# Performance work log

Hardware: AMD Instinct MI355X
Metric: run time of the kernel (lower is better)

## Reference

```python
import jax, jax.numpy as jnp
import numpy as np

D_MODEL = 1024
NUM_HEADS = 16
HEAD_SIZE = D_MODEL // NUM_HEADS


def setup_inputs() -> dict:
    key = jax.random.key(0)
    ks = jax.random.split(key, 11)
    B, S, D = 4, 2048, D_MODEL
    scale = 1.0 / np.sqrt(D)
    inp = {
        "queries": jax.random.normal(ks[0], (B, S, D), jnp.float32),
        "keys": jax.random.normal(ks[1], (B, S, D), jnp.float32),
        "values": jax.random.normal(ks[2], (B, S, D), jnp.float32),
        "W_Q": jax.random.normal(ks[3], (D, D), jnp.float32) * scale,
        "b_Q": jax.random.normal(ks[4], (D,), jnp.float32) * 0.01,
        "W_K": jax.random.normal(ks[5], (D, D), jnp.float32) * scale,
        "b_K": jax.random.normal(ks[6], (D,), jnp.float32) * 0.01,
        "W_V": jax.random.normal(ks[7], (D, D), jnp.float32) * scale,
        "b_V": jax.random.normal(ks[8], (D,), jnp.float32) * 0.01,
        "W_O": jax.random.normal(ks[9], (D, D), jnp.float32) * scale,
        "b_O": jax.random.normal(ks[10], (D,), jnp.float32) * 0.01,
    }
    return inp


def _split_heads(x):
    B, S, D = x.shape
    return x.reshape(B, S, NUM_HEADS, HEAD_SIZE).transpose(0, 2, 1, 3)  # (B,H,S,hd)


def reference(queries, keys, values, W_Q, b_Q, W_K, b_K, W_V, b_V, W_O, b_O):
    # Linear projections (torch Linear: x @ W^T + b; here W stored as (D,D) used directly)
    q = _split_heads(queries @ W_Q + b_Q)  # (B,H,S,hd)
    k = _split_heads(keys @ W_K + b_K)
    v = _split_heads(values @ W_V + b_V)

    S = q.shape[2]
    scores = jnp.einsum("bhqd,bhkd->bhqk", q, k) / jnp.sqrt(jnp.float32(HEAD_SIZE))
    causal = jnp.tril(jnp.ones((S, S), dtype=bool))  # True where attention allowed
    scores = jnp.where(causal, scores, -jnp.inf)
    attn = jax.nn.softmax(scores, axis=-1)  # (B,H,S,S)

    ctx = jnp.einsum("bhqk,bhkd->bhqd", attn, v)  # (B,H,S,hd)
    B = ctx.shape[0]
    ctx = ctx.transpose(0, 2, 1, 3).reshape(B, S, D_MODEL)  # merge heads
    out = ctx @ W_O + b_O
    return out, jax.lax.stop_gradient(attn)
```

## Files before the change

### kernel.cpp

```cpp
#include <hip/hip_runtime.h>
#include <hip/hip_bf16.h>
#include <math.h>

#define D_MODEL 1024
#define NUM_HEADS 16
#define HEAD_SIZE 64
#define SEQ 2048
#define BATCH 4
#define M_PROJ (BATCH * SEQ)

typedef __attribute__((ext_vector_type(8))) short bf16x8;
typedef __attribute__((ext_vector_type(4))) float f32x4;

__device__ inline float bf2f(ushort u) {
  return __uint_as_float(((unsigned int)u) << 16);
}
__device__ inline ushort f2bf(float x) {
  unsigned int b = __float_as_uint(x);
  b += 0x7fffu + ((b >> 16) & 1u);
  return (ushort)(b >> 16);
}

__device__ inline void gload_lds16(const void* g, void* l) {
  __builtin_amdgcn_global_load_lds(
      (const __attribute__((address_space(1))) void*)g,
      (__attribute__((address_space(3))) void*)l, 16, 0, 0);
}

__global__ __launch_bounds__(256) void split_kernel(
    const float* __restrict__ in, ushort* __restrict__ hi,
    ushort* __restrict__ lo, int n4) {
  for (int i = blockIdx.x * 256 + threadIdx.x; i < n4; i += gridDim.x * 256) {
    float4 v = reinterpret_cast<const float4*>(in)[i];
    const float xs[4] = {v.x, v.y, v.z, v.w};
    ushort hh[4], ll[4];
#pragma unroll
    for (int j = 0; j < 4; ++j) {
      hh[j] = f2bf(xs[j]);
      ll[j] = f2bf(xs[j] - bf2f(hh[j]));
    }
    ushort4 h4, l4;
    h4.x = hh[0]; h4.y = hh[1]; h4.z = hh[2]; h4.w = hh[3];
    l4.x = ll[0]; l4.y = ll[1]; l4.z = ll[2]; l4.w = ll[3];
    reinterpret_cast<ushort4*>(hi)[i] = h4;
    reinterpret_cast<ushort4*>(lo)[i] = l4;
  }
}

__global__ __launch_bounds__(256) void transpose_split_kernel(
    const float* __restrict__ W, ushort* __restrict__ tHi,
    ushort* __restrict__ tLo) {
  __shared__ float tile[64][65];
  const int kt = blockIdx.y << 6, nt = blockIdx.x << 6;
  const int tx = threadIdx.x & 15, ty = threadIdx.x >> 4;
#pragma unroll
  for (int u = 0; u < 4; ++u) {
    const int r = ty + (u << 4);
    float4 v = *reinterpret_cast<const float4*>(
        &W[(size_t)(kt + r) * D_MODEL + nt + (tx << 2)]);
    tile[r][(tx << 2) + 0] = v.x;
    tile[r][(tx << 2) + 1] = v.y;
    tile[r][(tx << 2) + 2] = v.z;
    tile[r][(tx << 2) + 3] = v.w;
  }
  __syncthreads();
#pragma unroll
  for (int u = 0; u < 4; ++u) {
    const int n = ty + (u << 4);
    ushort h[4], l[4];
#pragma unroll
    for (int i = 0; i < 4; ++i) {
      const float x = tile[(tx << 2) + i][n];
      h[i] = f2bf(x);
      l[i] = f2bf(x - bf2f(h[i]));
    }
    ushort4 h4, l4;
    h4.x = h[0]; h4.y = h[1]; h4.z = h[2]; h4.w = h[3];
    l4.x = l[0]; l4.y = l[1]; l4.z = l[2]; l4.w = l[3];
    *reinterpret_cast<ushort4*>(
        &tHi[(size_t)(nt + n) * D_MODEL + kt + (tx << 2)]) = h4;
    *reinterpret_cast<ushort4*>(
        &tLo[(size_t)(nt + n) * D_MODEL + kt + (tx << 2)]) = l4;
  }
}

__global__ __launch_bounds__(256) void mfma_gemm_kernel(
    const ushort* __restrict__ Ahi, const ushort* __restrict__ Alo,
    const ushort* __restrict__ Bhi, const ushort* __restrict__ Blo,
    const float* __restrict__ bias, float* __restrict__ C,
    int M, int N, int K) {
  __shared__ short lds[16384];
  const int tid = threadIdx.x;
  const int wid = tid >> 6, lane = tid & 63;

  const int nbn = N >> 7;
  const int cpx = gridDim.x >> 3;
  const int swz = (blockIdx.x & 7) * cpx + (blockIdx.x >> 3);
  const int bm = (swz / nbn) << 7;
  const int bn = (swz % nbn) << 7;

  const int rowoff = lane & 15;
  const int koff = (lane >> 4) << 3;
  const int wr = wid >> 1, wc = wid & 1;

  f32x4 acc[4][4] = {};

  for (int k0 = 0; k0 < K; k0 += 32) {
#pragma unroll
    for (int iss = 0; iss < 2; ++iss) {
      const int f = (iss << 2) + wid;
      const size_t arow = (size_t)(bm + f * 16 + rowoff) * K + k0 + koff;
      const size_t brow = (size_t)(bn + f * 16 + rowoff) * K + k0 + koff;
      gload_lds16(Ahi + arow, &lds[0 * 4096 + f * 512]);
      gload_lds16(Alo + arow, &lds[1 * 4096 + f * 512]);
      gload_lds16(Bhi + brow, &lds[2 * 4096 + f * 512]);
      gload_lds16(Blo + brow, &lds[3 * 4096 + f * 512]);
    }
    __syncthreads();

    bf16x8 ah[4], al[4], bh[4], bl[4];
#pragma unroll
    for (int i = 0; i < 4; ++i) {
      const int fa = wr * 4 + i;
      const int fb = wc * 4 + i;
      ah[i] = *reinterpret_cast<const bf16x8*>(&lds[0 * 4096 + fa * 512 + lane * 8]);
      al[i] = *reinterpret_cast<const bf16x8*>(&lds[1 * 4096 + fa * 512 + lane * 8]);
      bh[i] = *reinterpret_cast<const bf16x8*>(&lds[2 * 4096 + fb * 512 + lane * 8]);
      bl[i] = *reinterpret_cast<const bf16x8*>(&lds[3 * 4096 + fb * 512 + lane * 8]);
    }
#pragma unroll
    for (int mi = 0; mi < 4; ++mi)
#pragma unroll
      for (int ni = 0; ni < 4; ++ni) {
        acc[mi][ni] = __builtin_amdgcn_mfma_f32_16x16x32_bf16(
            ah[mi], bh[ni], acc[mi][ni], 0, 0, 0);
        acc[mi][ni] = __builtin_amdgcn_mfma_f32_16x16x32_bf16(
            ah[mi], bl[ni], acc[mi][ni], 0, 0, 0);
        acc[mi][ni] = __builtin_amdgcn_mfma_f32_16x16x32_bf16(
            al[mi], bh[ni], acc[mi][ni], 0, 0, 0);
      }
    __syncthreads();
  }

  const int crowbase = bm + wr * 64 + ((lane >> 4) << 2);
  const int ccolbase = bn + wc * 64 + (lane & 15);
#pragma unroll
  for (int ni = 0; ni < 4; ++ni) {
    const int col = ccolbase + ni * 16;
    const float bv = bias[col];
#pragma unroll
    for (int mi = 0; mi < 4; ++mi) {
      const int row = crowbase + mi * 16;
#pragma unroll
      for (int j = 0; j < 4; ++j)
        C[(size_t)(row + j) * N + col] = acc[mi][ni][j] + bv;
    }
  }
}

__global__ __launch_bounds__(256) void scores_mfma_kernel(
    const ushort* __restrict__ Qhi, const ushort* __restrict__ Qlo,
    const ushort* __restrict__ Khi, const ushort* __restrict__ Klo,
    float* __restrict__ attn) {
  __shared__ short lds[32768];
  const int tid = threadIdx.x;
  const int wid = tid >> 6, lane = tid & 63;
  const int bh = blockIdx.y;
  const int b = bh >> 4;
  const int h = bh & 15;
  const int t = blockIdx.x;
  int qt = (int)((sqrtf(8.f * (float)t + 1.f) - 1.f) * 0.5f);
  while ((qt * (qt + 1)) / 2 > t) --qt;
  while (((qt + 1) * (qt + 2)) / 2 <= t) ++qt;
  const int kt = t - (qt * (qt + 1)) / 2;

  const int rowoff = lane & 15;
  const int koff = (lane >> 4) << 3;
  const int wr = wid >> 1, wc = wid & 1;

  const size_t qbase = (size_t)(b * SEQ + qt * 128) * D_MODEL + h * 64;
  const size_t kbase = (size_t)(b * SEQ + kt * 128) * D_MODEL + h * 64;
#pragma unroll
  for (int iss = 0; iss < 2; ++iss) {
    const int f = (iss << 2) + wid;
#pragma unroll
    for (int s = 0; s < 2; ++s) {
      const size_t qa = qbase + (size_t)(f * 16 + rowoff) * D_MODEL + s * 32 + koff;
      const size_t ka = kbase + (size_t)(f * 16 + rowoff) * D_MODEL + s * 32 + koff;
      const int lo_ = (f * 2 + s) * 512;
      gload_lds16(Qhi + qa, &lds[0 * 8192 + lo_]);
      gload_lds16(Qlo + qa, &lds[1 * 8192 + lo_]);
      gload_lds16(Khi + ka, &lds[2 * 8192 + lo_]);
      gload_lds16(Klo + ka, &lds[3 * 8192 + lo_]);
    }
  }
  __syncthreads();

  f32x4 acc[4][4] = {};
#pragma unroll
  for (int s = 0; s < 2; ++s) {
    bf16x8 ah[4], al[4], kh[4], kl[4];
#pragma unroll
    for (int i = 0; i < 4; ++i) {
      const int fa = ((wr * 4 + i) * 2 + s) * 512 + lane * 8;
      const int fb = ((wc * 4 + i) * 2 + s) * 512 + lane * 8;
      ah[i] = *reinterpret_cast<const bf16x8*>(&lds[0 * 8192 + fa]);
      al[i] = *reinterpret_cast<const bf16x8*>(&lds[1 * 8192 + fa]);
      kh[i] = *reinterpret_cast<const bf16x8*>(&lds[2 * 8192 + fb]);
      kl[i] = *reinterpret_cast<const bf16x8*>(&lds[3 * 8192 + fb]);
    }
#pragma unroll
    for (int mi = 0; mi < 4; ++mi)
#pragma unroll
      for (int ni = 0; ni < 4; ++ni) {
        acc[mi][ni] = __builtin_amdgcn_mfma_f32_16x16x32_bf16(
            ah[mi], kh[ni], acc[mi][ni], 0, 0, 0);
        acc[mi][ni] = __builtin_amdgcn_mfma_f32_16x16x32_bf16(
            ah[mi], kl[ni], acc[mi][ni], 0, 0, 0);
        acc[mi][ni] = __builtin_amdgcn_mfma_f32_16x16x32_bf16(
            al[mi], kh[ni], acc[mi][ni], 0, 0, 0);
      }
  }

  const int crowbase = qt * 128 + wr * 64 + ((lane >> 4) << 2);
  const int ccolbase = kt * 128 + wc * 64 + (lane & 15);
#pragma unroll
  for (int ni = 0; ni < 4; ++ni) {
    const int col = ccolbase + ni * 16;
#pragma unroll
    for (int mi = 0; mi < 4; ++mi) {
      const int row = crowbase + mi * 16;
#pragma unroll
      for (int j = 0; j < 4; ++j)
        attn[((size_t)bh * SEQ + row + j) * SEQ + col] = acc[mi][ni][j] * 0.125f;
    }
  }
}

__global__ __launch_bounds__(256) void softmax_kernel(float* __restrict__ attn) {
  const size_t row = blockIdx.x;
  const int q = (int)(row & (SEQ - 1));
  const int n = q + 1;
  float* p = attn + row * (size_t)SEQ;
  const int tid = threadIdx.x;

  float v[8];
#pragma unroll
  for (int u = 0; u < 8; ++u) {
    const int i = tid + (u << 8);
    v[u] = (i < n) ? p[i] : -INFINITY;
  }
  float m = v[0];
#pragma unroll
  for (int u = 1; u < 8; ++u) m = fmaxf(m, v[u]);
#pragma unroll
  for (int off = 1; off < 64; off <<= 1) m = fmaxf(m, __shfl_xor(m, off, 64));
  __shared__ float redm[4];
  if ((tid & 63) == 0) redm[tid >> 6] = m;
  __syncthreads();
  m = fmaxf(fmaxf(redm[0], redm[1]), fmaxf(redm[2], redm[3]));

  float s = 0.f;
#pragma unroll
  for (int u = 0; u < 8; ++u) {
    const float e = expf(v[u] - m);
    v[u] = e;
    s += e;
  }
#pragma unroll
  for (int off = 1; off < 64; off <<= 1) s += __shfl_xor(s, off, 64);
  __shared__ float reds[4];
  if ((tid & 63) == 0) reds[tid >> 6] = s;
  __syncthreads();
  s = reds[0] + reds[1] + reds[2] + reds[3];

  const float inv = 1.f / s;
#pragma unroll
  for (int u = 0; u < 8; ++u) p[tid + (u << 8)] = v[u] * inv;
}

__global__ __launch_bounds__(256) void pv_kernel(
    const float* __restrict__ attn, const float* __restrict__ V,
    float* __restrict__ ctx) {
  const int qt = blockIdx.x;
  const int bh = blockIdx.y;
  const int b = bh >> 4;
  const int h = bh & 15;
  __shared__ float Ps[16][132];
  __shared__ float Vs[16][68];
  const int tid = threadIdx.x;
  const int tx = tid & 15;
  const int ty = tid >> 4;
  float acc[2][4][4] = {};

  const int kmax = (qt + 1) * 128;
  const float* arow = attn + ((size_t)bh * SEQ + qt * 128) * SEQ;
  const int pr = tid >> 2, pc = (tid & 3) << 2;
  const int vr = tid >> 4, vc = (tid & 15) << 2;

  for (int k0 = 0; k0 < kmax; k0 += 16) {
#pragma unroll
    for (int hh = 0; hh < 2; ++hh) {
      const int r = pr + hh * 64;
      float4 p4 =
          *reinterpret_cast<const float4*>(&arow[(size_t)r * SEQ + k0 + pc]);
      Ps[pc + 0][r] = p4.x; Ps[pc + 1][r] = p4.y;
      Ps[pc + 2][r] = p4.z; Ps[pc + 3][r] = p4.w;
    }
    float4 v4 = *reinterpret_cast<const float4*>(
        &V[(size_t)(b * SEQ + k0 + vr) * D_MODEL + h * 64 + vc]);
    *reinterpret_cast<float4*>(&Vs[vr][vc]) = v4;
    __syncthreads();
#pragma unroll
    for (int kk = 0; kk < 16; ++kk) {
      float4 a0 = *reinterpret_cast<const float4*>(&Ps[kk][ty << 2]);
      float4 a1 = *reinterpret_cast<const float4*>(&Ps[kk][64 + (ty << 2)]);
      float4 vv = *reinterpret_cast<const float4*>(&Vs[kk][tx << 2]);
      const float am[2][4] = {{a0.x, a0.y, a0.z, a0.w},
                              {a1.x, a1.y, a1.z, a1.w}};
      const float vn[4] = {vv.x, vv.y, vv.z, vv.w};
#pragma unroll
      for (int p = 0; p < 2; ++p)
#pragma unroll
        for (int i = 0; i < 4; ++i)
#pragma unroll
          for (int j = 0; j < 4; ++j)
            acc[p][i][j] += am[p][i] * vn[j];
    }
    __syncthreads();
  }

#pragma unroll
  for (int p = 0; p < 2; ++p)
#pragma unroll
    for (int i = 0; i < 4; ++i) {
      float4 o = {acc[p][i][0], acc[p][i][1], acc[p][i][2], acc[p][i][3]};
      *reinterpret_cast<float4*>(
          &ctx[(size_t)(b * SEQ + qt * 128 + p * 64 + (ty << 2) + i) *
                   D_MODEL + h * 64 + (tx << 2)]) = o;
    }
}

extern "C" void kernel_launch(void* const* d_in, const int* in_sizes, int n_in,
                              void* d_out, int out_size, void* d_ws,
                              size_t ws_size, hipStream_t stream) {
  const float* queries = (const float*)d_in[0];
  const float* keys = (const float*)d_in[1];
  const float* values = (const float*)d_in[2];
  const float* W_Q = (const float*)d_in[3];
  const float* b_Q = (const float*)d_in[4];
  const float* W_K = (const float*)d_in[5];
  const float* b_K = (const float*)d_in[6];
  const float* W_V = (const float*)d_in[7];
  const float* b_V = (const float*)d_in[8];
  const float* W_O = (const float*)d_in[9];
  const float* b_O = (const float*)d_in[10];

  float* out = (float*)d_out;
  float* attn = out + (size_t)BATCH * SEQ * D_MODEL;

  const size_t PE = (size_t)M_PROJ * D_MODEL;
  float* Q = (float*)d_ws;
  float* K = Q + PE;
  float* V = K + PE;
  float* ctx = V + PE;
  ushort* Xhi = (ushort*)(ctx + PE);
  ushort* Xlo = Xhi + PE;
  ushort* Wthi = Xlo + PE;
  ushort* Wtlo = Wthi + (size_t)D_MODEL * D_MODEL;
  ushort* Qhi = Wtlo + (size_t)D_MODEL * D_MODEL;
  ushort* Qlo = Qhi + PE;
  ushort* Khi = Qlo + PE;
  ushort* Klo = Khi + PE;

  const dim3 blk(256);
  const int n4 = (int)(PE / 4);

  auto do_gemm = [&](const float* X, const float* W, const float* b,
                     float* Cout) {
    split_kernel<<<2048, blk, 0, stream>>>(X, Xhi, Xlo, n4);
    transpose_split_kernel<<<dim3(16, 16), blk, 0, stream>>>(W, Wthi, Wtlo);
    mfma_gemm_kernel<<<dim3(512), blk, 0, stream>>>(
        Xhi, Xlo, Wthi, Wtlo, b, Cout, M_PROJ, D_MODEL, D_MODEL);
  };

  do_gemm(queries, W_Q, b_Q, Q);
  do_gemm(keys, W_K, b_K, K);
  do_gemm(values, W_V, b_V, V);

  split_kernel<<<2048, blk, 0, stream>>>(Q, Qhi, Qlo, n4);
  split_kernel<<<2048, blk, 0, stream>>>(K, Khi, Klo, n4);

  const int ntri = (SEQ / 128) * (SEQ / 128 + 1) / 2;
  scores_mfma_kernel<<<dim3(ntri, BATCH * NUM_HEADS), blk, 0, stream>>>(
      Qhi, Qlo, Khi, Klo, attn);

  softmax_kernel<<<dim3(BATCH * NUM_HEADS * SEQ), blk, 0, stream>>>(attn);

  pv_kernel<<<dim3(SEQ / 128, BATCH * NUM_HEADS), blk, 0, stream>>>(attn, V,
                                                                    ctx);

  do_gemm(ctx, W_O, b_O, out);
}
```

Before: 2.282 ms.

## Move PV product to bf16 MFMA and fuse hi/lo splits into GEMM epilogues

Replaces the FP32 scalar PV kernel with an MFMA kernel that reads a bf16 copy of the probabilities written by softmax and a transposed hi/lo split V produced directly by the V projection epilogue. The Q/K projections now emit hi/lo bf16 directly, and PV emits ctx hi/lo, which removes separate split passes and the FP32 Q/K/V/ctx buffers. In exchange, softmax writes an extra 2-byte-per-element P array (a large write), and P is used only as bf16 (hi part only), which lowers the accuracy of the PV product.

```diff
diff --git a/kernel.cpp b/kernel.cpp
--- a/kernel.cpp
+++ b/kernel.cpp
@@ -84,11 +84,12 @@
   }
 }
 
+template <int MODE>
 __global__ __launch_bounds__(256) void mfma_gemm_kernel(
     const ushort* __restrict__ Ahi, const ushort* __restrict__ Alo,
     const ushort* __restrict__ Bhi, const ushort* __restrict__ Blo,
-    const float* __restrict__ bias, float* __restrict__ C,
-    int M, int N, int K) {
+    const float* __restrict__ bias, float* __restrict__ Cf,
+    ushort* __restrict__ Chi, ushort* __restrict__ Clo, int M, int N, int K) {
   __shared__ short lds[16384];
   const int tid = threadIdx.x;
   const int wid = tid >> 6, lane = tid & 63;
@@ -150,10 +151,34 @@
     const float bv = bias[col];
 #pragma unroll
     for (int mi = 0; mi < 4; ++mi) {
-      const int row = crowbase + mi * 16;
-#pragma unroll
-      for (int j = 0; j < 4; ++j)
-        C[(size_t)(row + j) * N + col] = acc[mi][ni][j] + bv;
+      const int row0 = crowbase + mi * 16;
+      if constexpr (MODE == 0) {
+#pragma unroll
+        for (int j = 0; j < 4; ++j)
+          Cf[(size_t)(row0 + j) * N + col] = acc[mi][ni][j] + bv;
+      } else if constexpr (MODE == 1) {
+#pragma unroll
+        for (int j = 0; j < 4; ++j) {
+          const float v = acc[mi][ni][j] + bv;
+          const ushort h = f2bf(v);
+          Chi[(size_t)(row0 + j) * N + col] = h;
+          Clo[(size_t)(row0 + j) * N + col] = f2bf(v - bf2f(h));
+        }
+      } else {
+        ushort4 h4, l4;
+        ushort* hp = reinterpret_cast<ushort*>(&h4);
+        ushort* lp = reinterpret_cast<ushort*>(&l4);
+#pragma unroll
+        for (int j = 0; j < 4; ++j) {
+          const float v = acc[mi][ni][j] + bv;
+          hp[j] = f2bf(v);
+          lp[j] = f2bf(v - bf2f(hp[j]));
+        }
+        const size_t vt = ((size_t)((row0 >> 11) << 10) + col) * SEQ +
+                          (row0 & (SEQ - 1));
+        *reinterpret_cast<ushort4*>(&Chi[vt]) = h4;
+        *reinterpret_cast<ushort4*>(&Clo[vt]) = l4;
+      }
     }
   }
 }
@@ -237,11 +262,13 @@
   }
 }
 
-__global__ __launch_bounds__(256) void softmax_kernel(float* __restrict__ attn) {
+__global__ __launch_bounds__(256) void softmax_kernel(
+    float* __restrict__ attn, ushort* __restrict__ Pout) {
   const size_t row = blockIdx.x;
   const int q = (int)(row & (SEQ - 1));
   const int n = q + 1;
   float* p = attn + row * (size_t)SEQ;
+  ushort* pb = Pout + row * (size_t)SEQ;
   const int tid = threadIdx.x;
 
   float v[8];
@@ -276,69 +303,87 @@
 
   const float inv = 1.f / s;
 #pragma unroll
-  for (int u = 0; u < 8; ++u) p[tid + (u << 8)] = v[u] * inv;
-}
-
-__global__ __launch_bounds__(256) void pv_kernel(
-    const float* __restrict__ attn, const float* __restrict__ V,
-    float* __restrict__ ctx) {
+  for (int u = 0; u < 8; ++u) {
+    const float pv = v[u] * inv;
+    p[tid + (u << 8)] = pv;
+    pb[tid + (u << 8)] = f2bf(pv);
+  }
+}
+
+__global__ __launch_bounds__(256) void pv_mfma_kernel(
+    const ushort* __restrict__ P, const ushort* __restrict__ Vthi,
+    const ushort* __restrict__ Vtlo, ushort* __restrict__ ctxHi,
+    ushort* __restrict__ ctxLo) {
+  __shared__ short lds[8192];
+  const int tid = threadIdx.x;
+  const int wid = tid >> 6, lane = tid & 63;
   const int qt = blockIdx.x;
   const int bh = blockIdx.y;
   const int b = bh >> 4;
   const int h = bh & 15;
-  __shared__ float Ps[16][132];
-  __shared__ float Vs[16][68];
-  const int tid = threadIdx.x;
-  const int tx = tid & 15;
-  const int ty = tid >> 4;
-  float acc[2][4][4] = {};
-
+
+  const int rowoff = lane & 15;
+  const int koff = (lane >> 4) << 3;
+  const int wr = wid >> 1, wc = wid & 1;
+
+  const size_t pbase = (size_t)bh * SEQ * SEQ + (size_t)(qt * 128) * SEQ;
+  const size_t vbase = (size_t)bh * 64 * SEQ;
+
+  f32x4 acc[4][2] = {};
   const int kmax = (qt + 1) * 128;
-  const float* arow = attn + ((size_t)bh * SEQ + qt * 128) * SEQ;
-  const int pr = tid >> 2, pc = (tid & 3) << 2;
-  const int vr = tid >> 4, vc = (tid & 15) << 2;
-
-  for (int k0 = 0; k0 < kmax; k0 += 16) {
-#pragma unroll
-    for (int hh = 0; hh < 2; ++hh) {
-      const int r = pr + hh * 64;
-      float4 p4 =
-          *reinterpret_cast<const float4*>(&arow[(size_t)r * SEQ + k0 + pc]);
-      Ps[pc + 0][r] = p4.x; Ps[pc + 1][r] = p4.y;
-      Ps[pc + 2][r] = p4.z; Ps[pc + 3][r] = p4.w;
-    }
-    float4 v4 = *reinterpret_cast<const float4*>(
-        &V[(size_t)(b * SEQ + k0 + vr) * D_MODEL + h * 64 + vc]);
-    *reinterpret_cast<float4*>(&Vs[vr][vc]) = v4;
+
+  for (int k0 = 0; k0 < kmax; k0 += 32) {
+#pragma unroll
+    for (int u = 0; u < 2; ++u) {
+      const int f = 2 * wid + u;
+      const size_t pa = pbase + (size_t)(f * 16 + rowoff) * SEQ + k0 + koff;
+      gload_lds16(P + pa, &lds[f * 512]);
+    }
+    const size_t va = vbase + (size_t)(wid * 16 + rowoff) * SEQ + k0 + koff;
+    gload_lds16(Vthi + va, &lds[4096 + wid * 512]);
+    gload_lds16(Vtlo + va, &lds[6144 + wid * 512]);
     __syncthreads();
-#pragma unroll
-    for (int kk = 0; kk < 16; ++kk) {
-      float4 a0 = *reinterpret_cast<const float4*>(&Ps[kk][ty << 2]);
-      float4 a1 = *reinterpret_cast<const float4*>(&Ps[kk][64 + (ty << 2)]);
-      float4 vv = *reinterpret_cast<const float4*>(&Vs[kk][tx << 2]);
-      const float am[2][4] = {{a0.x, a0.y, a0.z, a0.w},
-                              {a1.x, a1.y, a1.z, a1.w}};
-      const float vn[4] = {vv.x, vv.y, vv.z, vv.w};
-#pragma unroll
-      for (int p = 0; p < 2; ++p)
-#pragma unroll
-        for (int i = 0; i < 4; ++i)
-#pragma unroll
-          for (int j = 0; j < 4; ++j)
-            acc[p][i][j] += am[p][i] * vn[j];
-    }
+
+    bf16x8 a[4], bhf[2], blf[2];
+#pragma unroll
+    for (int i = 0; i < 4; ++i)
+      a[i] = *reinterpret_cast<const bf16x8*>(&lds[(wr * 4 + i) * 512 + lane * 8]);
+#pragma unroll
+    for (int i = 0; i < 2; ++i) {
+      bhf[i] = *reinterpret_cast<const bf16x8*>(
+          &lds[4096 + (wc * 2 + i) * 512 + lane * 8]);
+      blf[i] = *reinterpret_cast<const bf16x8*>(
+          &lds[6144 + (wc * 2 + i) * 512 + lane * 8]);
+    }
+#pragma unroll
+    for (int mi = 0; mi < 4; ++mi)
+#pragma unroll
+      for (int ni = 0; ni < 2; ++ni) {
+        acc[mi][ni] = __builtin_amdgcn_mfma_f32_16x16x32_bf16(
+            a[mi], bhf[ni], acc[mi][ni], 0, 0, 0);
+        acc[mi][ni] = __builtin_amdgcn_mfma_f32_16x16x32_bf16(
+            a[mi], blf[ni], acc[mi][ni], 0, 0, 0);
+      }
     __syncthreads();
   }
 
-#pragma unroll
-  for (int p = 0; p < 2; ++p)
-#pragma unroll
-    for (int i = 0; i < 4; ++i) {
-      float4 o = {acc[p][i][0], acc[p][i][1], acc[p][i][2], acc[p][i][3]};
-      *reinterpret_cast<float4*>(
-          &ctx[(size_t)(b * SEQ + qt * 128 + p * 64 + (ty << 2) + i) *
-                   D_MODEL + h * 64 + (tx << 2)]) = o;
-    }
+  const int crowbase = qt * 128 + wr * 64 + ((lane >> 4) << 2);
+  const int ccolbase = h * 64 + wc * 32 + (lane & 15);
+#pragma unroll
+  for (int ni = 0; ni < 2; ++ni) {
+    const int col = ccolbase + ni * 16;
+#pragma unroll
+    for (int mi = 0; mi < 4; ++mi) {
+      const int row0 = b * SEQ + crowbase + mi * 16;
+#pragma unroll
+      for (int j = 0; j < 4; ++j) {
+        const float v = acc[mi][ni][j];
+        const ushort hi = f2bf(v);
+        ctxHi[(size_t)(row0 + j) * D_MODEL + col] = hi;
+        ctxLo[(size_t)(row0 + j) * D_MODEL + col] = f2bf(v - bf2f(hi));
+      }
+    }
+  }
 }
 
 extern "C" void kernel_launch(void* const* d_in, const int* in_sizes, int n_in,
@@ -360,45 +405,51 @@
   float* attn = out + (size_t)BATCH * SEQ * D_MODEL;
 
   const size_t PE = (size_t)M_PROJ * D_MODEL;
-  float* Q = (float*)d_ws;
-  float* K = Q + PE;
-  float* V = K + PE;
-  float* ctx = V + PE;
-  ushort* Xhi = (ushort*)(ctx + PE);
+  const size_t D2 = (size_t)D_MODEL * D_MODEL;
+  ushort* Xhi = (ushort*)d_ws;
   ushort* Xlo = Xhi + PE;
   ushort* Wthi = Xlo + PE;
-  ushort* Wtlo = Wthi + (size_t)D_MODEL * D_MODEL;
-  ushort* Qhi = Wtlo + (size_t)D_MODEL * D_MODEL;
+  ushort* Wtlo = Wthi + D2;
+  ushort* Qhi = Wtlo + D2;
   ushort* Qlo = Qhi + PE;
   ushort* Khi = Qlo + PE;
   ushort* Klo = Khi + PE;
+  ushort* Vthi = Klo + PE;
+  ushort* Vtlo = Vthi + PE;
+  ushort* ctxHi = Vtlo + PE;
+  ushort* ctxLo = ctxHi + PE;
+  ushort* Phi = ctxLo + PE;
 
   const dim3 blk(256);
   const int n4 = (int)(PE / 4);
-
-  auto do_gemm = [&](const float* X, const float* W, const float* b,
-                     float* Cout) {
-    split_kernel<<<2048, blk, 0, stream>>>(X, Xhi, Xlo, n4);
-    transpose_split_kernel<<<dim3(16, 16), blk, 0, stream>>>(W, Wthi, Wtlo);
-    mfma_gemm_kernel<<<dim3(512), blk, 0, stream>>>(
-        Xhi, Xlo, Wthi, Wtlo, b, Cout, M_PROJ, D_MODEL, D_MODEL);
-  };
-
-  do_gemm(queries, W_Q, b_Q, Q);
-  do_gemm(keys, W_K, b_K, K);
-  do_gemm(values, W_V, b_V, V);
-
-  split_kernel<<<2048, blk, 0, stream>>>(Q, Qhi, Qlo, n4);
-  split_kernel<<<2048, blk, 0, stream>>>(K, Khi, Klo, n4);
+  const dim3 ggemm(512);
+
+  split_kernel<<<2048, blk, 0, stream>>>(queries, Xhi, Xlo, n4);
+  transpose_split_kernel<<<dim3(16, 16), blk, 0, stream>>>(W_Q, Wthi, Wtlo);
+  mfma_gemm_kernel<1><<<ggemm, blk, 0, stream>>>(
+      Xhi, Xlo, Wthi, Wtlo, b_Q, nullptr, Qhi, Qlo, M_PROJ, D_MODEL, D_MODEL);
+
+  split_kernel<<<2048, blk, 0, stream>>>(keys, Xhi, Xlo, n4);
+  transpose_split_kernel<<<dim3(16, 16), blk, 0, stream>>>(W_K, Wthi, Wtlo);
+  mfma_gemm_kernel<1><<<ggemm, blk, 0, stream>>>(
+      Xhi, Xlo, Wthi, Wtlo, b_K, nullptr, Khi, Klo, M_PROJ, D_MODEL, D_MODEL);
+
+  split_kernel<<<2048, blk, 0, stream>>>(values, Xhi, Xlo, n4);
+  transpose_split_kernel<<<dim3(16, 16), blk, 0, stream>>>(W_V, Wthi, Wtlo);
+  mfma_gemm_kernel<2><<<ggemm, blk, 0, stream>>>(
+      Xhi, Xlo, Wthi, Wtlo, b_V, nullptr, Vthi, Vtlo, M_PROJ, D_MODEL, D_MODEL);
 
   const int ntri = (SEQ / 128) * (SEQ / 128 + 1) / 2;
   scores_mfma_kernel<<<dim3(ntri, BATCH * NUM_HEADS), blk, 0, stream>>>(
       Qhi, Qlo, Khi, Klo, attn);
 
-  softmax_kernel<<<dim3(BATCH * NUM_HEADS * SEQ), blk, 0, stream>>>(attn);
-
-  pv_kernel<<<dim3(SEQ / 128, BATCH * NUM_HEADS), blk, 0, stream>>>(attn, V,
-                                                                    ctx);
-
-  do_gemm(ctx, W_O, b_O, out);
-}
+  softmax_kernel<<<dim3(BATCH * NUM_HEADS * SEQ), blk, 0, stream>>>(attn, Phi);
+
+  pv_mfma_kernel<<<dim3(SEQ / 128, BATCH * NUM_HEADS), blk, 0, stream>>>(
+      Phi, Vthi, Vtlo, ctxHi, ctxLo);
+
+  transpose_split_kernel<<<dim3(16, 16), blk, 0, stream>>>(W_O, Wthi, Wtlo);
+  mfma_gemm_kernel<0><<<ggemm, blk, 0, stream>>>(
+      ctxHi, ctxLo, Wthi, Wtlo, b_O, out, nullptr, nullptr, M_PROJ, D_MODEL,
+      D_MODEL);
+}
```

New measurement: 2.181 ms. 4.5% less time.
